# Optimization experiments

Measured on AMD Instinct MI355X. Metric: run time of the kernel, lower is better.

The kernel has to match this reference:

```python
import jax, jax.numpy as jnp
import numpy as np

B, N, D, C, ND = 32, 196, 512, 500, 51  # batch, patches, embed dim, classes, 1+50 descriptions


def _l2norm(x):
    return x / jnp.linalg.norm(x, axis=-1, keepdims=True)


def setup_inputs() -> dict:
    key = jax.random.key(0)
    k1, k2, k3, k4 = jax.random.split(key, 4)
    all_text = _l2norm(jax.random.normal(k3, (ND, C, D), jnp.float32))
    return {
        "image_features": _l2norm(jax.random.normal(k1, (B, D), jnp.float32)),
        "local_image_features": _l2norm(jax.random.normal(k2, (B, N, D), jnp.float32)),
        "all_text_features": all_text,
        "mean_text_features": _l2norm(jnp.mean(all_text, axis=0)),
        "topk": 50,
    }


def reference(image_features, local_image_features, all_text_features, mean_text_features, topk):
    # Faithful translation of get_dense_logits2 (m==1 global-feature axis squeezed out).
    base_logits = image_features @ mean_text_features.T                       # [B, C]
    # w[b,n] = <global image feat b, local patch feat n>
    w = jnp.einsum('bd,bnd->bn', image_features, local_image_features)        # [B, N]
    # v[nd,c]: softmax over descriptions of <mean text c, description nd of class c>
    v = jax.nn.softmax(
        jnp.einsum('cd,ncd->nc', mean_text_features, all_text_features), axis=0)  # [ND, C]
    # sim[b,c,nd,m] = <patch m of image b, description nd of class c>
    sim = jnp.einsum('bmd,ncd->bcnm', local_image_features, all_text_features)    # [B, C, ND, N]
    vals, idx = jax.lax.top_k(sim, topk)                                      # [B, C, ND, k] over patch axis
    sim_top = jnp.swapaxes(vals, 2, 3)                                        # [B, C, k, ND]
    # torch: idx[:, 0, :, 0] -> class 0, description 0, all k indices
    sel = idx[:, 0, 0, :]                                                     # [B, k]
    wg = jax.nn.softmax(jnp.take_along_axis(w, sel, axis=1), axis=-1)         # [B, k]
    # weight[b,c,m,n] = wg[b,m] * v[n,c]
    weight = wg[:, None, :, None] * jnp.swapaxes(v, 0, 1)[None, :, None, :]   # [B, C, k, ND]
    bias_logits = jnp.sum(sim_top * weight, axis=(-2, -1))                    # [B, C]
    return base_logits + bias_logits
```

## Files before the change

### kernel.cpp

```cpp
#include <hip/hip_runtime.h>

#define B_ 32
#define N_ 196
#define D_ 512
#define C_ 500
#define ND_ 51

typedef __attribute__((ext_vector_type(8))) short short8_t;
typedef __attribute__((ext_vector_type(4))) unsigned short us4_t;
typedef __attribute__((ext_vector_type(4))) float f32x4;

typedef const __attribute__((address_space(1))) unsigned int* gas_p;
typedef __attribute__((address_space(3))) unsigned int* las_p;
#define GLDS(gp, lp) __builtin_amdgcn_global_load_lds((gas_p)(gp), (las_p)(lp), 16, 0, 0)

__device__ inline unsigned short f2bf(float f) {
    unsigned u = __float_as_uint(f);
    u += 0x7FFFu + ((u >> 16) & 1u);
    return (unsigned short)(u >> 16);
}

template <int CTRL>
__device__ inline float dpp_mov(float x) {
    return __uint_as_float(__builtin_amdgcn_update_dpp(
        __float_as_uint(x), __float_as_uint(x), CTRL, 0xF, 0xF, true));
}
__device__ inline float rsum64(float v) {
    v += dpp_mov<0x121>(v);
    v += dpp_mov<0x122>(v);
    v += dpp_mov<0x124>(v);
    v += dpp_mov<0x128>(v);
    v += __shfl_xor(v, 16);
    v += __shfl_xor(v, 32);
    return v;
}
__device__ inline float rmax64(float v) {
    v = fmaxf(v, dpp_mov<0x121>(v));
    v = fmaxf(v, dpp_mov<0x122>(v));
    v = fmaxf(v, dpp_mov<0x124>(v));
    v = fmaxf(v, dpp_mov<0x128>(v));
    v = fmaxf(v, __shfl_xor(v, 16));
    v = fmaxf(v, __shfl_xor(v, 32));
    return v;
}
template <int S>
__device__ inline float xsh(float y) {
    if constexpr (S == 1) return dpp_mov<0xB1>(y);
    else if constexpr (S == 2) return dpp_mov<0x4E>(y);
    else if constexpr (S == 8) return dpp_mov<0x128>(y);
    else return __shfl_xor(y, S);
}

__global__ __launch_bounds__(256) void k_ctd(const float* __restrict__ text,
                                             const float* __restrict__ mean,
                                             unsigned short* __restrict__ textbf,
                                             float* __restrict__ dots) {
    const int row = blockIdx.x * 4 + (threadIdx.x >> 6);
    const int lane = threadIdx.x & 63;
    const int n = row / C_;
    const int ccol = row - n * C_;
    const float* tp = text + (size_t)row * 512 + lane * 8;
    const float* mp = mean + (size_t)ccol * 512 + lane * 8;
    const float4 f0 = *(const float4*)tp;
    const float4 f1 = *(const float4*)(tp + 4);
    const float4 m0 = *(const float4*)mp;
    const float4 m1 = *(const float4*)(mp + 4);
    float a = f0.x * m0.x + f0.y * m0.y + f0.z * m0.z + f0.w * m0.w
            + f1.x * m1.x + f1.y * m1.y + f1.z * m1.z + f1.w * m1.w;
    a = rsum64(a);
    const us4_t p0 = {f2bf(f0.x), f2bf(f0.y), f2bf(f0.z), f2bf(f0.w)};
    const us4_t p1 = {f2bf(f1.x), f2bf(f1.y), f2bf(f1.z), f2bf(f1.w)};
    *(us4_t*)&textbf[(size_t)row * 512 + lane * 8] = p0;
    *(us4_t*)&textbf[(size_t)row * 512 + lane * 8 + 4] = p1;
    if (lane == 0) dots[row] = a;
}

__global__ __launch_bounds__(64) void k_vsm(const float* __restrict__ dots,
                                            float* __restrict__ vout) {
    const int c = blockIdx.x;
    const int lane = threadIdx.x;
    float xv = (lane < ND_) ? dots[lane * C_ + c] : -INFINITY;
    float mx = rmax64(xv);
    float e = (lane < ND_) ? expf(xv - mx) : 0.f;
    float sum = rsum64(e);
    if (lane < ND_) vout[lane * C_ + c] = e / sum;
}

__global__ __launch_bounds__(256) void k_cls(const float* __restrict__ image,
                                             const float* __restrict__ localf,
                                             const float* __restrict__ text,
                                             unsigned short* __restrict__ localbf,
                                             float* __restrict__ s_ws,
                                             float* __restrict__ wm_ws) {
    const int row = blockIdx.x * 4 + (threadIdx.x >> 6);
    const int lane = threadIdx.x & 63;
    const int b = row / N_;
    const float* lp = localf + (size_t)row * 512 + lane * 8;
    const float4 l0 = *(const float4*)lp;
    const float4 l1 = *(const float4*)(lp + 4);
    const float* ip = image + b * 512 + lane * 8;
    const float* t0p = text + lane * 8;
    const float4 i0 = *(const float4*)ip, i1 = *(const float4*)(ip + 4);
    const float4 t0 = *(const float4*)t0p, t1 = *(const float4*)(t0p + 4);
    float a = l0.x * t0.x + l0.y * t0.y + l0.z * t0.z + l0.w * t0.w
            + l1.x * t1.x + l1.y * t1.y + l1.z * t1.z + l1.w * t1.w;
    float g = l0.x * i0.x + l0.y * i0.y + l0.z * i0.z + l0.w * i0.w
            + l1.x * i1.x + l1.y * i1.y + l1.z * i1.z + l1.w * i1.w;
    a = rsum64(a);
    g = rsum64(g);
    const us4_t p0 = {f2bf(l0.x), f2bf(l0.y), f2bf(l0.z), f2bf(l0.w)};
    const us4_t p1 = {f2bf(l1.x), f2bf(l1.y), f2bf(l1.z), f2bf(l1.w)};
    *(us4_t*)&localbf[(size_t)row * 512 + lane * 8] = p0;
    *(us4_t*)&localbf[(size_t)row * 512 + lane * 8 + 4] = p1;
    if (lane == 0) { s_ws[row] = a; wm_ws[row] = g; }
}

__global__ __launch_bounds__(256) void k_v(const float* __restrict__ mean,
                                           const float* __restrict__ text,
                                           float* __restrict__ vout) {
    const int c = blockIdx.x;
    const int w = threadIdx.x >> 6, lane = threadIdx.x & 63;
    __shared__ float sc[ND_];
    float md[8];
#pragma unroll
    for (int t = 0; t < 8; ++t) md[t] = mean[c * 512 + lane + 64 * t];
    for (int j = 0; j < 13; ++j) {
        const int n = w + 4 * j;
        if (n < ND_) {
            const float* tp = &text[((size_t)n * C_ + c) * 512];
            float a = 0.f;
#pragma unroll
            for (int t = 0; t < 8; ++t) a += md[t] * tp[lane + 64 * t];
            a = rsum64(a);
            if (lane == 0) sc[n] = a;
        }
    }
    __syncthreads();
    if (w == 0) {
        float xv = (lane < ND_) ? sc[lane] : -INFINITY;
        float mx = rmax64(xv);
        float e = (lane < ND_) ? expf(xv - mx) : 0.f;
        float sum = rsum64(e);
        if (lane < ND_) vout[lane * C_ + c] = e / sum;
    }
}

__global__ __launch_bounds__(256) void k_sw(const float* __restrict__ image,
                                            const float* __restrict__ localf,
                                            const float* __restrict__ text,
                                            float* __restrict__ s_ws,
                                            float* __restrict__ wm_ws) {
    const int b = blockIdx.x;
    const int m0 = blockIdx.y * 28;
    const int w = threadIdx.x >> 6, lane = threadIdx.x & 63;
    float t00[8], img[8];
#pragma unroll
    for (int t = 0; t < 8; ++t) {
        t00[t] = text[lane + 64 * t];
        img[t] = image[b * 512 + lane + 64 * t];
    }
    for (int t7 = 0; t7 < 7; ++t7) {
        const int m = m0 + w * 7 + t7;
        const float* lp = &localf[((size_t)b * N_ + m) * 512];
        float a = 0.f, g = 0.f;
#pragma unroll
        for (int t = 0; t < 8; ++t) {
            const float lv = lp[lane + 64 * t];
            a += t00[t] * lv;
            g += img[t] * lv;
        }
        a = rsum64(a);
        g = rsum64(g);
        if (lane == 0) { s_ws[b * N_ + m] = a; wm_ws[b * N_ + m] = g; }
    }
}

__global__ __launch_bounds__(64) void k_sel(const float* __restrict__ s_ws,
                                            const float* __restrict__ wm_ws,
                                            float* __restrict__ wgout) {
    const int b = blockIdx.x;
    const int lane = threadIdx.x;
    const unsigned long long ltmask = (1ull << lane) - 1ull;
    __shared__ float cv[64], cw[64];

    float x[4], p[4];
#pragma unroll
    for (int i = 0; i < 4; ++i) {
        const int m = lane + 64 * i;
        x[i] = (m < N_) ? s_ws[b * N_ + m] : -INFINITY;
        p[i] = (m < N_) ? wm_ws[b * N_ + m] : 0.f;
    }
    float lo = -1.02f, hi = 1.02f;
    int cl = N_;
    for (int it = 0; it < 24; ++it) {
        const float t = 0.5f * (lo + hi);
        int cnum = 0;
#pragma unroll
        for (int i = 0; i < 4; ++i) cnum += __popcll(__ballot(x[i] > t));
        if (cnum >= 50) { lo = t; cl = cnum; if (cnum <= 64) break; }
        else hi = t;
    }
    bool f[4];
    if (cl <= 64) {
#pragma unroll
        for (int i = 0; i < 4; ++i) f[i] = x[i] > lo;
    } else {
        int s1 = 0;
#pragma unroll
        for (int i = 0; i < 4; ++i) s1 += __popcll(__ballot(x[i] > hi));
        const int need = 64 - s1;
        int run = 0;
#pragma unroll
        for (int i = 0; i < 4; ++i) {
            const bool mid = (x[i] > lo) && !(x[i] > hi);
            const unsigned long long bm = __ballot(mid);
            const int pos = run + __popcll(bm & ltmask);
            f[i] = (x[i] > hi) || (mid && pos < need);
            run += __popcll(bm);
        }
    }
    int basep = 0;
#pragma unroll
    for (int i = 0; i < 4; ++i) {
        const unsigned long long bm = __ballot(f[i]);
        const int pos = basep + __popcll(bm & ltmask);
        if (f[i]) { cv[pos] = x[i]; cw[pos] = p[i]; }
        basep += __popcll(bm);
    }
    __builtin_amdgcn_s_waitcnt(0);
    float y = (lane < basep) ? cv[lane] : -INFINITY;
    float z = (lane < basep) ? cw[lane] : 0.f;
#pragma unroll
    for (int k = 2; k <= 64; k <<= 1) {
#pragma unroll
        for (int s2 = k >> 1; s2 > 0; s2 >>= 1) {
            const float py = __shfl_xor(y, s2);
            const float pz = __shfl_xor(z, s2);
            const bool keep_max = ((lane & k) == 0) == ((lane & s2) == 0);
            const bool take = keep_max ? (py > y) : (py < y);
            if (take) { y = py; z = pz; }
        }
    }
    float xv = (lane < 50) ? z : -INFINITY;
    float mx = xv;
#pragma unroll
    for (int off = 32; off; off >>= 1) mx = fmaxf(mx, __shfl_xor(mx, off));
    float e = (lane < 50) ? expf(xv - mx) : 0.f;
    float sum = e;
#pragma unroll
    for (int off = 32; off; off >>= 1) sum += __shfl_xor(sum, off);
    if (lane < 50) wgout[b * 50 + lane] = e / sum;
}

#define BSTEP(S, UP) { \
    const float q1 = xsh<S>(y1); \
    const float q2 = xsh<S>(y2); \
    if ((q1 > y1) == (UP)) y1 = q1; \
    if ((q2 > y2) == (UP)) y2 = q2; }

__global__ __launch_bounds__(512, 6) void k_main(const float* __restrict__ image,
                                                 const float* __restrict__ mean,
                                                 const unsigned short* __restrict__ localbf,
                                                 const unsigned short* __restrict__ textbf,
                                                 const float* __restrict__ vws,
                                                 const float* __restrict__ wgws,
                                                 float* __restrict__ out) {
    const int b = blockIdx.x;
    const int c = blockIdx.y;
    const int tid = threadIdx.x;
    const int w = tid >> 6;
    const int lane = tid & 63;
    const int quad = lane >> 4;
    const int l16 = lane & 15;

    __shared__ __align__(16) union SU {
        unsigned short stg[ND_ * 196 * 2];
        float ST[ND_ * 196];
    } u;

    float base_reg = 0.f;
    if (w == 0) {
        float s = 0.f;
#pragma unroll
        for (int t = 0; t < 8; ++t)
            s += image[b * 512 + lane + 64 * t] * mean[c * 512 + lane + 64 * t];
        s = rsum64(s);
        base_reg = s;
    }

    f32x4 acc[2][4];
    const f32x4 zv = {0.f, 0.f, 0.f, 0.f};
#pragma unroll
    for (int i = 0; i < 2; ++i)
#pragma unroll
        for (int j = 0; j < 4; ++j) acc[i][j] = zv;

    const unsigned short* abase = localbf + (size_t)(b * N_) * 512;

    for (int ks = 0; ks < 8; ++ks) {
#pragma unroll
        for (int i = 0; i < 4; ++i) {
            const int s = i * 512 + tid;
            if (s < 1568) {
                const int r = s >> 3;
                const int c8 = (s & 7) ^ (r & 7);
                GLDS(abase + (size_t)r * 512 + ks * 64 + c8 * 8, (char*)u.stg + s * 16);
            }
        }
        {
            const int s = tid;
            if (s < 408) {
                const int r = s >> 3;
                const int c8 = (s & 7) ^ (r & 7);
                GLDS(textbf + (size_t)(r * C_ + c) * 512 + ks * 64 + c8 * 8,
                     (char*)u.stg + 25088 + s * 16);
            }
        }
        __syncthreads();
#pragma unroll
        for (int kc = 0; kc < 2; ++kc) {
            short8_t bfr[4];
#pragma unroll
            for (int nt = 0; nt < 4; ++nt) {
                const int row = nt * 16 + l16;
                const int j = kc * 4 + quad;
                bfr[nt] = *(const short8_t*)&u.stg[12544 + row * 64 + ((j ^ (row & 7)) * 8)];
            }
#pragma unroll
            for (int mi = 0; mi < 2; ++mi) {
                const int mt = w + 8 * mi;
                if (mt < 13) {
                    const int row = mt * 16 + l16;
                    const int j = kc * 4 + quad;
                    short8_t af = *(const short8_t*)&u.stg[row * 64 + ((j ^ (row & 7)) * 8)];
#pragma unroll
                    for (int nt = 0; nt < 4; ++nt)
                        acc[mi][nt] = __builtin_amdgcn_mfma_f32_16x16x32_bf16(af, bfr[nt], acc[mi][nt], 0, 0, 0);
                }
            }
        }
        __syncthreads();
    }

#pragma unroll
    for (int nt = 0; nt < 4; ++nt) {
        const int n = nt * 16 + l16;
        if (n < ND_) {
#pragma unroll
            for (int mi = 0; mi < 2; ++mi) {
                const int mt = w + 8 * mi;
                if (mt < 12 || (mt == 12 && quad == 0))
                    *(f32x4*)&u.ST[n * 196 + mt * 16 + quad * 4] = acc[mi][nt];
            }
        }
    }
    __syncthreads();

    const float wgv = (lane < 50) ? wgws[b * 50 + lane] : 0.f;
    const unsigned long long ltmask = (1ull << lane) - 1ull;
    float waveacc = 0.f;

    const bool L0 = (lane & 1) == 0, L1 = (lane & 2) == 0, L2 = (lane & 4) == 0,
               L3 = (lane & 8) == 0, L4 = (lane & 16) == 0, L5 = (lane & 32) == 0;

    for (int t = 0; t < 4; ++t) {
        const int n1 = w + 16 * t;
        const int n2 = n1 + 8;
        const bool a2 = (n2 < ND_);
        if (n1 >= ND_) break;
        float* rowp1 = &u.ST[n1 * 196];
        float* rowp2 = &u.ST[(a2 ? n2 : n1) * 196];

        float x1[4], x2[4];
        if (lane < 49) {
            f32x4 v1 = *(const f32x4*)&rowp1[lane * 4];
            f32x4 v2 = *(const f32x4*)&rowp2[lane * 4];
#pragma unroll
            for (int r = 0; r < 4; ++r) { x1[r] = v1[r]; x2[r] = a2 ? v2[r] : -INFINITY; }
        } else {
#pragma unroll
            for (int r = 0; r < 4; ++r) { x1[r] = -INFINITY; x2[r] = -INFINITY; }
        }

        float lo1 = -1.02f, hi1 = 1.02f, lo2 = -1.02f, hi2 = 1.02f;
        int cl1 = 256, cl2 = a2 ? 256 : 0;
        bool d1 = false, d2 = !a2;
        for (int it = 0; it < 24 && !(d1 && d2); ++it) {
            const float t1 = 0.5f * (lo1 + hi1);
            const float t2 = 0.5f * (lo2 + hi2);
            int c1 = 0, c2 = 0;
#pragma unroll
            for (int i = 0; i < 4; ++i) {
                c1 += __popcll(__ballot(x1[i] > t1));
                c2 += __popcll(__ballot(x2[i] > t2));
            }
            if (!d1) { if (c1 >= 50) { lo1 = t1; cl1 = c1; d1 = (c1 <= 64); } else hi1 = t1; }
            if (!d2) { if (c2 >= 50) { lo2 = t2; cl2 = c2; d2 = (c2 <= 64); } else hi2 = t2; }
        }

        bool f1[4], f2[4];
        int cnt1, cnt2;
        if (cl1 <= 64) {
#pragma unroll
            for (int i = 0; i < 4; ++i) f1[i] = x1[i] > lo1;
            cnt1 = cl1;
        } else {
            int s1 = 0;
#pragma unroll
            for (int i = 0; i < 4; ++i) s1 += __popcll(__ballot(x1[i] > hi1));
            const int need = 64 - s1;
            int run = 0;
#pragma unroll
            for (int i = 0; i < 4; ++i) {
                const bool mid = (x1[i] > lo1) && !(x1[i] > hi1);
                const unsigned long long bm = __ballot(mid);
                const int pos = run + __popcll(bm & ltmask);
                f1[i] = (x1[i] > hi1) || (mid && pos < need);
                run += __popcll(bm);
            }
            cnt1 = 64;
        }
        if (cl2 <= 64) {
#pragma unroll
            for (int i = 0; i < 4; ++i) f2[i] = x2[i] > lo2;
            cnt2 = cl2;
        } else {
            int s1 = 0;
#pragma unroll
            for (int i = 0; i < 4; ++i) s1 += __popcll(__ballot(x2[i] > hi2));
            const int need = 64 - s1;
            int run = 0;
#pragma unroll
            for (int i = 0; i < 4; ++i) {
                const bool mid = (x2[i] > lo2) && !(x2[i] > hi2);
                const unsigned long long bm = __ballot(mid);
                const int pos = run + __popcll(bm & ltmask);
                f2[i] = (x2[i] > hi2) || (mid && pos < need);
                run += __popcll(bm);
            }
            cnt2 = 64;
        }

        int bp1 = 0, bp2 = 0;
#pragma unroll
        for (int i = 0; i < 4; ++i) {
            const unsigned long long bm1 = __ballot(f1[i]);
            const unsigned long long bm2 = __ballot(f2[i]);
            const int p1 = bp1 + __popcll(bm1 & ltmask);
            const int p2 = bp2 + __popcll(bm2 & ltmask);
            if (f1[i]) rowp1[p1] = x1[i];
            if (f2[i]) rowp2[p2] = x2[i];
            bp1 += __popcll(bm1);
            bp2 += __popcll(bm2);
        }
        __builtin_amdgcn_s_waitcnt(0);
        float y1 = (lane < cnt1) ? rowp1[lane] : -INFINITY;
        float y2 = (lane < cnt2) ? rowp2[lane] : -INFINITY;

        BSTEP(1, L1 == L0)
        BSTEP(2, L2 == L1) BSTEP(1, L2 == L0)
        BSTEP(4, L3 == L2) BSTEP(2, L3 == L1) BSTEP(1, L3 == L0)
        BSTEP(8, L4 == L3) BSTEP(4, L4 == L2) BSTEP(2, L4 == L1) BSTEP(1, L4 == L0)
        BSTEP(16, L5 == L4) BSTEP(8, L5 == L3) BSTEP(4, L5 == L2) BSTEP(2, L5 == L1) BSTEP(1, L5 == L0)
        BSTEP(32, L5) BSTEP(16, L4) BSTEP(8, L3) BSTEP(4, L2) BSTEP(2, L1) BSTEP(1, L0)

        float part1 = (lane < 50) ? y1 * wgv : 0.f;
        float part2 = (lane < 50) ? y2 * wgv : 0.f;
        part1 = rsum64(part1);
        part2 = rsum64(part2);
        waveacc += vws[n1 * C_ + c] * part1;
        if (a2) waveacc += vws[n2 * C_ + c] * part2;
    }

    if (lane == 0) u.ST[w * 196] = waveacc;
    __syncthreads();
    if (tid == 0) {
        float r = base_reg;
#pragma unroll
        for (int i = 0; i < 8; ++i) r += u.ST[i * 196];
        out[b * C_ + c] = r;
    }
}

__global__ __launch_bounds__(256) void k_main_fb(const float* __restrict__ image,
                                                 const float* __restrict__ localf,
                                                 const float* __restrict__ text,
                                                 const float* __restrict__ mean,
                                                 const float* __restrict__ vws,
                                                 const float* __restrict__ wgws,
                                                 float* __restrict__ out) {
    const int c = blockIdx.x;
    const int b = blockIdx.y;
    const int tid = threadIdx.x;
    const int w = tid >> 6;
    const int lane = tid & 63;
    const int quad = lane >> 4;
    const int l16 = lane & 15;

    __shared__ __align__(16) union SU {
        struct { unsigned short A[208 * 72]; unsigned short Bm[64 * 72]; } st;
        float S[208 * 65];
    } u;
    __shared__ float wavepart[4];
    __shared__ float basev;

    if (w == 0) {
        float s = 0.f;
#pragma unroll
        for (int t = 0; t < 8; ++t)
            s += image[b * 512 + lane + 64 * t] * mean[c * 512 + lane + 64 * t];
#pragma unroll
        for (int off = 32; off; off >>= 1) s += __shfl_xor(s, off);
        if (lane == 0) basev = s;
    }

    f32x4 acc[4][4];
    const f32x4 zv = {0.f, 0.f, 0.f, 0.f};
#pragma unroll
    for (int i = 0; i < 4; ++i)
#pragma unroll
        for (int j = 0; j < 4; ++j) acc[i][j] = zv;

    const int lbase = (b * N_) * 512;
    for (int ks = 0; ks < 8; ++ks) {
        const int k0 = ks * 64;
        for (int e = tid; e < 3328; e += 256) {
            const int m = e >> 4, kc4 = e & 15;
            float4 fv = make_float4(0.f, 0.f, 0.f, 0.f);
            if (m < N_) fv = *(const float4*)&localf[lbase + m * 512 + k0 + kc4 * 4];
            us4_t pk = {f2bf(fv.x), f2bf(fv.y), f2bf(fv.z), f2bf(fv.w)};
            *(us4_t*)&u.st.A[m * 72 + kc4 * 4] = pk;
        }
        for (int e = tid; e < 1024; e += 256) {
            const int n = e >> 4, kc4 = e & 15;
            float4 fv = make_float4(0.f, 0.f, 0.f, 0.f);
            if (n < ND_) fv = *(const float4*)&text[((size_t)n * C_ + c) * 512 + k0 + kc4 * 4];
            us4_t pk = {f2bf(fv.x), f2bf(fv.y), f2bf(fv.z), f2bf(fv.w)};
            *(us4_t*)&u.st.Bm[n * 72 + kc4 * 4] = pk;
        }
        __syncthreads();
#pragma unroll
        for (int kc = 0; kc < 2; ++kc) {
            short8_t bfr[4];
#pragma unroll
            for (int nt = 0; nt < 4; ++nt)
                bfr[nt] = *(const short8_t*)&u.st.Bm[(nt * 16 + l16) * 72 + kc * 32 + quad * 8];
#pragma unroll
            for (int mi = 0; mi < 4; ++mi) {
                const int mt = w + 4 * mi;
                if (mt < 13) {
                    short8_t af = *(const short8_t*)&u.st.A[(mt * 16 + l16) * 72 + kc * 32 + quad * 8];
#pragma unroll
                    for (int nt = 0; nt < 4; ++nt)
                        acc[mi][nt] = __builtin_amdgcn_mfma_f32_16x16x32_bf16(af, bfr[nt], acc[mi][nt], 0, 0, 0);
                }
            }
        }
        __syncthreads();
    }

#pragma unroll
    for (int mi = 0; mi < 4; ++mi) {
        const int mt = w + 4 * mi;
        if (mt < 13) {
#pragma unroll
            for (int nt = 0; nt < 4; ++nt)
#pragma unroll
                for (int r = 0; r < 4; ++r)
                    u.S[(mt * 16 + quad * 4 + r) * 65 + nt * 16 + l16] = acc[mi][nt][r];
        }
    }
    __syncthreads();

    const float wgv = (lane < 50) ? wgws[b * 50 + lane] : 0.f;
    float waveacc = 0.f;

    for (int j = 0; j < 13; ++j) {
        const int n = w + 4 * j;
        if (n < ND_) {
            float x[4];
#pragma unroll
            for (int i = 0; i < 4; ++i) {
                const int m = lane + 64 * i;
                x[i] = (m < N_) ? u.S[m * 65 + n] : -INFINITY;
            }
#pragma unroll
            for (int k = 2; k <= 64; k <<= 1) {
#pragma unroll
                for (int s2 = k >> 1; s2 > 0; s2 >>= 1) {
                    const bool up = ((lane & k) == 0) == ((lane & s2) == 0);
#pragma unroll
                    for (int r = 0; r < 4; ++r) {
                        const float p = __shfl_xor(x[r], s2);
                        x[r] = up ? fmaxf(x[r], p) : fminf(x[r], p);
                    }
                }
            }
            float m01 = fmaxf(x[0], __shfl_xor(x[1], 63));
            float m23 = fmaxf(x[2], __shfl_xor(x[3], 63));
#pragma unroll
            for (int s2 = 32; s2 > 0; s2 >>= 1) {
                const bool up = (lane & s2) == 0;
                const float p0 = __shfl_xor(m01, s2);
                const float p1 = __shfl_xor(m23, s2);
                m01 = up ? fmaxf(m01, p0) : fminf(m01, p0);
                m23 = up ? fmaxf(m23, p1) : fminf(m23, p1);
            }
            float y = fmaxf(m01, __shfl_xor(m23, 63));
#pragma unroll
            for (int s2 = 32; s2 > 0; s2 >>= 1) {
                const bool up = (lane & s2) == 0;
                const float p = __shfl_xor(y, s2);
                y = up ? fmaxf(y, p) : fminf(y, p);
            }
            float part = (lane < 50) ? y * wgv : 0.f;
#pragma unroll
            for (int off = 32; off; off >>= 1) part += __shfl_xor(part, off);
            waveacc += vws[n * C_ + c] * part;
        }
    }

    if (lane == 0) wavepart[w] = waveacc;
    __syncthreads();
    if (tid == 0)
        out[b * C_ + c] = basev + wavepart[0] + wavepart[1] + wavepart[2] + wavepart[3];
}

extern "C" void kernel_launch(void* const* d_in, const int* in_sizes, int n_in,
                              void* d_out, int out_size, void* d_ws, size_t ws_size,
                              hipStream_t stream) {
    (void)in_sizes; (void)n_in; (void)out_size;
    const float* image = (const float*)d_in[0];
    const float* localf = (const float*)d_in[1];
    const float* text  = (const float*)d_in[2];
    const float* mean  = (const float*)d_in[3];
    float* out = (float*)d_out;

    float* vws   = (float*)d_ws;
    float* wgws  = vws + ND_ * C_;
    float* s_ws  = wgws + B_ * 50;
    float* wm_ws = s_ws + B_ * N_;
    float* dots  = wm_ws + B_ * N_;
    const size_t small_bytes = (size_t)(2 * ND_ * C_ + B_ * 50 + 2 * B_ * N_) * 4;
    const size_t bf_bytes = ((size_t)B_ * N_ * D_ + (size_t)ND_ * C_ * D_) * 2;

    if (ws_size >= small_bytes + bf_bytes) {
        unsigned short* localbf = (unsigned short*)(dots + ND_ * C_);
        unsigned short* textbf  = localbf + (size_t)B_ * N_ * D_;
        hipLaunchKernelGGL(k_ctd, dim3(ND_ * C_ / 4), dim3(256), 0, stream,
                           text, mean, textbf, dots);
        hipLaunchKernelGGL(k_vsm, dim3(C_), dim3(64), 0, stream, dots, vws);
        hipLaunchKernelGGL(k_cls, dim3(B_ * N_ / 4), dim3(256), 0, stream,
                           image, localf, text, localbf, s_ws, wm_ws);
        hipLaunchKernelGGL(k_sel, dim3(B_), dim3(64), 0, stream, s_ws, wm_ws, wgws);
        hipLaunchKernelGGL(k_main, dim3(B_, C_), dim3(512), 0, stream,
                           image, mean, localbf, textbf, vws, wgws, out);
    } else {
        hipLaunchKernelGGL(k_v, dim3(C_), dim3(256), 0, stream, mean, text, vws);
        hipLaunchKernelGGL(k_sw, dim3(B_, 7), dim3(256), 0, stream, image, localf, text, s_ws, wm_ws);
        hipLaunchKernelGGL(k_sel, dim3(B_), dim3(64), 0, stream, s_ws, wm_ws, wgws);
        hipLaunchKernelGGL(k_main_fb, dim3(C_, B_), dim3(256), 0, stream,
                           image, localf, text, mean, vws, wgws, out);
    }
}
```

Baseline: 638.6 us.

## Process two classes per k_main block to reuse staged local-patch tiles

Each k_main block now computes two classes instead of one. The staged bf16 local-feature tile is loaded once and used for both classes' MFMA accumulations, which halves the redundant global loads of local features and halves the grid. In exchange it doubles accumulator registers (occupancy hint lowered from 6 to 4), uses more LDS staging, and runs the top-k phase twice in sequence with an extra barrier.

```diff
diff --git a/kernel.cpp b/kernel.cpp
--- a/kernel.cpp
+++ b/kernel.cpp
@@ -258,7 +258,7 @@
     if ((q1 > y1) == (UP)) y1 = q1; \
     if ((q2 > y2) == (UP)) y2 = q2; }
 
-__global__ __launch_bounds__(512, 6) void k_main(const float* __restrict__ image,
+__global__ __launch_bounds__(512, 4) void k_main(const float* __restrict__ image,
                                                  const float* __restrict__ mean,
                                                  const unsigned short* __restrict__ localbf,
                                                  const unsigned short* __restrict__ textbf,
@@ -266,7 +266,8 @@
                                                  const float* __restrict__ wgws,
                                                  float* __restrict__ out) {
     const int b = blockIdx.x;
-    const int c = blockIdx.y;
+    const int c0 = blockIdx.y * 2;
+    const int c1 = c0 + 1;
     const int tid = threadIdx.x;
     const int w = tid >> 6;
     const int lane = tid & 63;
@@ -278,22 +279,25 @@
         float ST[ND_ * 196];
     } u;
 
-    float base_reg = 0.f;
+    float base0 = 0.f, base1 = 0.f;
     if (w == 0) {
-        float s = 0.f;
-#pragma unroll
-        for (int t = 0; t < 8; ++t)
-            s += image[b * 512 + lane + 64 * t] * mean[c * 512 + lane + 64 * t];
-        s = rsum64(s);
-        base_reg = s;
-    }
-
-    f32x4 acc[2][4];
+        float s0 = 0.f, s1 = 0.f;
+#pragma unroll
+        for (int t = 0; t < 8; ++t) {
+            const float iv = image[b * 512 + lane + 64 * t];
+            s0 += iv * mean[c0 * 512 + lane + 64 * t];
+            s1 += iv * mean[c1 * 512 + lane + 64 * t];
+        }
+        base0 = rsum64(s0);
+        base1 = rsum64(s1);
+    }
+
+    f32x4 acc0[2][4], acc1[2][4];
     const f32x4 zv = {0.f, 0.f, 0.f, 0.f};
 #pragma unroll
     for (int i = 0; i < 2; ++i)
 #pragma unroll
-        for (int j = 0; j < 4; ++j) acc[i][j] = zv;
+        for (int j = 0; j < 4; ++j) { acc0[i][j] = zv; acc1[i][j] = zv; }
 
     const unsigned short* abase = localbf + (size_t)(b * N_) * 512;
 
@@ -307,178 +311,194 @@
                 GLDS(abase + (size_t)r * 512 + ks * 64 + c8 * 8, (char*)u.stg + s * 16);
             }
         }
-        {
-            const int s = tid;
-            if (s < 408) {
-                const int r = s >> 3;
-                const int c8 = (s & 7) ^ (r & 7);
-                GLDS(textbf + (size_t)(r * C_ + c) * 512 + ks * 64 + c8 * 8,
-                     (char*)u.stg + 25088 + s * 16);
+#pragma unroll
+        for (int i = 0; i < 2; ++i) {
+            const int q = i * 512 + tid;
+            if (q < 816) {
+                const int cc = (q < 408) ? c0 : c1;
+                const int ql = (q < 408) ? q : q - 408;
+                const int r = ql >> 3;
+                const int c8 = (ql & 7) ^ (r & 7);
+                GLDS(textbf + (size_t)(r * C_ + cc) * 512 + ks * 64 + c8 * 8,
+                     (char*)u.stg + 25088 + q * 16);
             }
         }
         __syncthreads();
 #pragma unroll
         for (int kc = 0; kc < 2; ++kc) {
-            short8_t bfr[4];
-#pragma unroll
-            for (int nt = 0; nt < 4; ++nt) {
-                const int row = nt * 16 + l16;
-                const int j = kc * 4 + quad;
-                bfr[nt] = *(const short8_t*)&u.stg[12544 + row * 64 + ((j ^ (row & 7)) * 8)];
-            }
-#pragma unroll
-            for (int mi = 0; mi < 2; ++mi) {
-                const int mt = w + 8 * mi;
-                if (mt < 13) {
-                    const int row = mt * 16 + l16;
+#pragma unroll
+            for (int cph = 0; cph < 2; ++cph) {
+                f32x4 (&accC)[2][4] = cph ? acc1 : acc0;
+                const int bbase = 12544 + cph * 3264;
+                short8_t bfr[4];
+#pragma unroll
+                for (int nt = 0; nt < 4; ++nt) {
+                    const int row = nt * 16 + l16;
                     const int j = kc * 4 + quad;
-                    short8_t af = *(const short8_t*)&u.stg[row * 64 + ((j ^ (row & 7)) * 8)];
-#pragma unroll
-                    for (int nt = 0; nt < 4; ++nt)
-                        acc[mi][nt] = __builtin_amdgcn_mfma_f32_16x16x32_bf16(af, bfr[nt], acc[mi][nt], 0, 0, 0);
+                    bfr[nt] = *(const short8_t*)&u.stg[bbase + row * 64 + ((j ^ (row & 7)) * 8)];
+                }
+#pragma unroll
+                for (int mi = 0; mi < 2; ++mi) {
+                    const int mt = w + 8 * mi;
+                    if (mt < 13) {
+                        const int row = mt * 16 + l16;
+                        const int j = kc * 4 + quad;
+                        short8_t af = *(const short8_t*)&u.stg[row * 64 + ((j ^ (row & 7)) * 8)];
+#pragma unroll
+                        for (int nt = 0; nt < 4; ++nt)
+                            accC[mi][nt] = __builtin_amdgcn_mfma_f32_16x16x32_bf16(af, bfr[nt], accC[mi][nt], 0, 0, 0);
+                    }
                 }
             }
         }
         __syncthreads();
     }
-
-#pragma unroll
-    for (int nt = 0; nt < 4; ++nt) {
-        const int n = nt * 16 + l16;
-        if (n < ND_) {
-#pragma unroll
-            for (int mi = 0; mi < 2; ++mi) {
-                const int mt = w + 8 * mi;
-                if (mt < 12 || (mt == 12 && quad == 0))
-                    *(f32x4*)&u.ST[n * 196 + mt * 16 + quad * 4] = acc[mi][nt];
-            }
-        }
-    }
-    __syncthreads();
 
     const float wgv = (lane < 50) ? wgws[b * 50 + lane] : 0.f;
     const unsigned long long ltmask = (1ull << lane) - 1ull;
-    float waveacc = 0.f;
-
     const bool L0 = (lane & 1) == 0, L1 = (lane & 2) == 0, L2 = (lane & 4) == 0,
                L3 = (lane & 8) == 0, L4 = (lane & 16) == 0, L5 = (lane & 32) == 0;
-
-    for (int t = 0; t < 4; ++t) {
-        const int n1 = w + 16 * t;
-        const int n2 = n1 + 8;
-        const bool a2 = (n2 < ND_);
-        if (n1 >= ND_) break;
-        float* rowp1 = &u.ST[n1 * 196];
-        float* rowp2 = &u.ST[(a2 ? n2 : n1) * 196];
-
-        float x1[4], x2[4];
-        if (lane < 49) {
-            f32x4 v1 = *(const f32x4*)&rowp1[lane * 4];
-            f32x4 v2 = *(const f32x4*)&rowp2[lane * 4];
-#pragma unroll
-            for (int r = 0; r < 4; ++r) { x1[r] = v1[r]; x2[r] = a2 ? v2[r] : -INFINITY; }
-        } else {
-#pragma unroll
-            for (int r = 0; r < 4; ++r) { x1[r] = -INFINITY; x2[r] = -INFINITY; }
-        }
-
-        float lo1 = -1.02f, hi1 = 1.02f, lo2 = -1.02f, hi2 = 1.02f;
-        int cl1 = 256, cl2 = a2 ? 256 : 0;
-        bool d1 = false, d2 = !a2;
-        for (int it = 0; it < 24 && !(d1 && d2); ++it) {
-            const float t1 = 0.5f * (lo1 + hi1);
-            const float t2 = 0.5f * (lo2 + hi2);
-            int c1 = 0, c2 = 0;
+    float wa0 = 0.f, wa1 = 0.f;
+
+#pragma unroll
+    for (int ph = 0; ph < 2; ++ph) {
+        if (ph == 1) __syncthreads();
+        const int cc = ph ? c1 : c0;
+
+#pragma unroll
+        for (int nt = 0; nt < 4; ++nt) {
+            const int n = nt * 16 + l16;
+            if (n < ND_) {
+#pragma unroll
+                for (int mi = 0; mi < 2; ++mi) {
+                    const int mt = w + 8 * mi;
+                    if (mt < 12 || (mt == 12 && quad == 0))
+                        *(f32x4*)&u.ST[n * 196 + mt * 16 + quad * 4] = ph ? acc1[mi][nt] : acc0[mi][nt];
+                }
+            }
+        }
+        __syncthreads();
+
+        float waveacc = 0.f;
+        for (int t = 0; t < 4; ++t) {
+            const int n1 = w + 16 * t;
+            const int n2 = n1 + 8;
+            const bool a2 = (n2 < ND_);
+            if (n1 >= ND_) break;
+            float* rowp1 = &u.ST[n1 * 196];
+            float* rowp2 = &u.ST[(a2 ? n2 : n1) * 196];
+
+            float x1[4], x2[4];
+            if (lane < 49) {
+                f32x4 v1 = *(const f32x4*)&rowp1[lane * 4];
+                f32x4 v2 = *(const f32x4*)&rowp2[lane * 4];
+#pragma unroll
+                for (int r = 0; r < 4; ++r) { x1[r] = v1[r]; x2[r] = a2 ? v2[r] : -INFINITY; }
+            } else {
+#pragma unroll
+                for (int r = 0; r < 4; ++r) { x1[r] = -INFINITY; x2[r] = -INFINITY; }
+            }
+
+            float lo1 = -1.02f, hi1 = 1.02f, lo2 = -1.02f, hi2 = 1.02f;
+            int cl1 = 256, cl2 = a2 ? 256 : 0;
+            bool d1 = false, d2 = !a2;
+            for (int it = 0; it < 24 && !(d1 && d2); ++it) {
+                const float t1 = 0.5f * (lo1 + hi1);
+                const float t2 = 0.5f * (lo2 + hi2);
+                int cn1 = 0, cn2 = 0;
+#pragma unroll
+                for (int i = 0; i < 4; ++i) {
+                    cn1 += __popcll(__ballot(x1[i] > t1));
+                    cn2 += __popcll(__ballot(x2[i] > t2));
+                }
+                if (!d1) { if (cn1 >= 50) { lo1 = t1; cl1 = cn1; d1 = (cn1 <= 64); } else hi1 = t1; }
+                if (!d2) { if (cn2 >= 50) { lo2 = t2; cl2 = cn2; d2 = (cn2 <= 64); } else hi2 = t2; }
+            }
+
+            bool f1[4], f2[4];
+            int cnt1, cnt2;
+            if (cl1 <= 64) {
+#pragma unroll
+                for (int i = 0; i < 4; ++i) f1[i] = x1[i] > lo1;
+                cnt1 = cl1;
+            } else {
+                int s1 = 0;
+#pragma unroll
+                for (int i = 0; i < 4; ++i) s1 += __popcll(__ballot(x1[i] > hi1));
+                const int need = 64 - s1;
+                int run = 0;
+#pragma unroll
+                for (int i = 0; i < 4; ++i) {
+                    const bool mid = (x1[i] > lo1) && !(x1[i] > hi1);
+                    const unsigned long long bm = __ballot(mid);
+                    const int pos = run + __popcll(bm & ltmask);
+                    f1[i] = (x1[i] > hi1) || (mid && pos < need);
+                    run += __popcll(bm);
+                }
+                cnt1 = 64;
+            }
+            if (cl2 <= 64) {
+#pragma unroll
+                for (int i = 0; i < 4; ++i) f2[i] = x2[i] > lo2;
+                cnt2 = cl2;
+            } else {
+                int s1 = 0;
+#pragma unroll
+                for (int i = 0; i < 4; ++i) s1 += __popcll(__ballot(x2[i] > hi2));
+                const int need = 64 - s1;
+                int run = 0;
+#pragma unroll
+                for (int i = 0; i < 4; ++i) {
+                    const bool mid = (x2[i] > lo2) && !(x2[i] > hi2);
+                    const unsigned long long bm = __ballot(mid);
+                    const int pos = run + __popcll(bm & ltmask);
+                    f2[i] = (x2[i] > hi2) || (mid && pos < need);
+                    run += __popcll(bm);
+                }
+                cnt2 = 64;
+            }
+
+            int bp1 = 0, bp2 = 0;
 #pragma unroll
             for (int i = 0; i < 4; ++i) {
-                c1 += __popcll(__ballot(x1[i] > t1));
-                c2 += __popcll(__ballot(x2[i] > t2));
-            }
-            if (!d1) { if (c1 >= 50) { lo1 = t1; cl1 = c1; d1 = (c1 <= 64); } else hi1 = t1; }
-            if (!d2) { if (c2 >= 50) { lo2 = t2; cl2 = c2; d2 = (c2 <= 64); } else hi2 = t2; }
-        }
-
-        bool f1[4], f2[4];
-        int cnt1, cnt2;
-        if (cl1 <= 64) {
-#pragma unroll
-            for (int i = 0; i < 4; ++i) f1[i] = x1[i] > lo1;
-            cnt1 = cl1;
-        } else {
-            int s1 = 0;
-#pragma unroll
-            for (int i = 0; i < 4; ++i) s1 += __popcll(__ballot(x1[i] > hi1));
-            const int need = 64 - s1;
-            int run = 0;
-#pragma unroll
-            for (int i = 0; i < 4; ++i) {
-                const bool mid = (x1[i] > lo1) && !(x1[i] > hi1);
-                const unsigned long long bm = __ballot(mid);
-                const int pos = run + __popcll(bm & ltmask);
-                f1[i] = (x1[i] > hi1) || (mid && pos < need);
-                run += __popcll(bm);
-            }
-            cnt1 = 64;
-        }
-        if (cl2 <= 64) {
-#pragma unroll
-            for (int i = 0; i < 4; ++i) f2[i] = x2[i] > lo2;
-            cnt2 = cl2;
-        } else {
-            int s1 = 0;
-#pragma unroll
-            for (int i = 0; i < 4; ++i) s1 += __popcll(__ballot(x2[i] > hi2));
-            const int need = 64 - s1;
-            int run = 0;
-#pragma unroll
-            for (int i = 0; i < 4; ++i) {
-                const bool mid = (x2[i] > lo2) && !(x2[i] > hi2);
-                const unsigned long long bm = __ballot(mid);
-                const int pos = run + __popcll(bm & ltmask);
-                f2[i] = (x2[i] > hi2) || (mid && pos < need);
-                run += __popcll(bm);
-            }
-            cnt2 = 64;
-        }
-
-        int bp1 = 0, bp2 = 0;
-#pragma unroll
-        for (int i = 0; i < 4; ++i) {
-            const unsigned long long bm1 = __ballot(f1[i]);
-            const unsigned long long bm2 = __ballot(f2[i]);
-            const int p1 = bp1 + __popcll(bm1 & ltmask);
-            const int p2 = bp2 + __popcll(bm2 & ltmask);
-            if (f1[i]) rowp1[p1] = x1[i];
-            if (f2[i]) rowp2[p2] = x2[i];
-            bp1 += __popcll(bm1);
-            bp2 += __popcll(bm2);
-        }
-        __builtin_amdgcn_s_waitcnt(0);
-        float y1 = (lane < cnt1) ? rowp1[lane] : -INFINITY;
-        float y2 = (lane < cnt2) ? rowp2[lane] : -INFINITY;
-
-        BSTEP(1, L1 == L0)
-        BSTEP(2, L2 == L1) BSTEP(1, L2 == L0)
-        BSTEP(4, L3 == L2) BSTEP(2, L3 == L1) BSTEP(1, L3 == L0)
-        BSTEP(8, L4 == L3) BSTEP(4, L4 == L2) BSTEP(2, L4 == L1) BSTEP(1, L4 == L0)
-        BSTEP(16, L5 == L4) BSTEP(8, L5 == L3) BSTEP(4, L5 == L2) BSTEP(2, L5 == L1) BSTEP(1, L5 == L0)
-        BSTEP(32, L5) BSTEP(16, L4) BSTEP(8, L3) BSTEP(4, L2) BSTEP(2, L1) BSTEP(1, L0)
-
-        float part1 = (lane < 50) ? y1 * wgv : 0.f;
-        float part2 = (lane < 50) ? y2 * wgv : 0.f;
-        part1 = rsum64(part1);
-        part2 = rsum64(part2);
-        waveacc += vws[n1 * C_ + c] * part1;
-        if (a2) waveacc += vws[n2 * C_ + c] * part2;
-    }
-
-    if (lane == 0) u.ST[w * 196] = waveacc;
+                const unsigned long long bm1 = __ballot(f1[i]);
+                const unsigned long long bm2 = __ballot(f2[i]);
+                const int p1 = bp1 + __popcll(bm1 & ltmask);
+                const int p2 = bp2 + __popcll(bm2 & ltmask);
+                if (f1[i]) rowp1[p1] = x1[i];
+                if (f2[i]) rowp2[p2] = x2[i];
+                bp1 += __popcll(bm1);
+                bp2 += __popcll(bm2);
+            }
+            __builtin_amdgcn_s_waitcnt(0);
+            float y1 = (lane < cnt1) ? rowp1[lane] : -INFINITY;
+            float y2 = (lane < cnt2) ? rowp2[lane] : -INFINITY;
+
+            BSTEP(1, L1 == L0)
+            BSTEP(2, L2 == L1) BSTEP(1, L2 == L0)
+            BSTEP(4, L3 == L2) BSTEP(2, L3 == L1) BSTEP(1, L3 == L0)
+            BSTEP(8, L4 == L3) BSTEP(4, L4 == L2) BSTEP(2, L4 == L1) BSTEP(1, L4 == L0)
+            BSTEP(16, L5 == L4) BSTEP(8, L5 == L3) BSTEP(4, L5 == L2) BSTEP(2, L5 == L1) BSTEP(1, L5 == L0)
+            BSTEP(32, L5) BSTEP(16, L4) BSTEP(8, L3) BSTEP(4, L2) BSTEP(2, L1) BSTEP(1, L0)
+
+            float part1 = (lane < 50) ? y1 * wgv : 0.f;
+            float part2 = (lane < 50) ? y2 * wgv : 0.f;
+            part1 = rsum64(part1);
+            part2 = rsum64(part2);
+            waveacc += vws[n1 * C_ + cc] * part1;
+            if (a2) waveacc += vws[n2 * C_ + cc] * part2;
+        }
+        if (ph == 0) wa0 = waveacc; else wa1 = waveacc;
+    }
+
+    if (lane == 0) { u.ST[w * 196] = wa0; u.ST[w * 196 + 1] = wa1; }
     __syncthreads();
     if (tid == 0) {
-        float r = base_reg;
-#pragma unroll
-        for (int i = 0; i < 8; ++i) r += u.ST[i * 196];
-        out[b * C_ + c] = r;
+        float r0 = base0, r1 = base1;
+#pragma unroll
+        for (int i = 0; i < 8; ++i) { r0 += u.ST[i * 196]; r1 += u.ST[i * 196 + 1]; }
+        out[b * C_ + c0] = r0;
+        out[b * C_ + c1] = r1;
     }
 }
 
@@ -653,7 +673,7 @@
         hipLaunchKernelGGL(k_cls, dim3(B_ * N_ / 4), dim3(256), 0, stream,
                            image, localf, text, localbf, s_ws, wm_ws);
         hipLaunchKernelGGL(k_sel, dim3(B_), dim3(64), 0, stream, s_ws, wm_ws, wgws);
-        hipLaunchKernelGGL(k_main, dim3(B_, C_), dim3(512), 0, stream,
+        hipLaunchKernelGGL(k_main, dim3(B_, C_ / 2), dim3(512), 0, stream,
                            image, mean, localbf, textbf, vws, wgws, out);
     } else {
         hipLaunchKernelGGL(k_v, dim3(C_), dim3(256), 0, stream, mean, text, vws);
```

After: 713.1 us. +11.7%, slower.
